# Performance work log

Hardware: AMD Instinct MI355X
Metric: run time of the kernel (lower is better)

## Reference

```python
import jax, jax.numpy as jnp
import numpy as np

NUM_CP = 64
D_MODEL = 128
N = 1_000_000


def setup_inputs() -> dict:
    key = jax.random.key(0)
    k_t, k_cp = jax.random.split(key)
    t = jax.random.uniform(k_t, (N,), dtype=jnp.float32)  # in [0,1)
    control_points = jax.random.normal(k_cp, (NUM_CP, D_MODEL), dtype=jnp.float32) / np.sqrt(NUM_CP)
    return {"t": t, "control_points": control_points}


def reference(t, control_points):
    # Faithful to the torch loop:
    #   out = sum_{i=0}^{K-2} (1 - |t - i|) * cp[i]
    # Note: weights are NOT clamped to >=0 in the original, so we keep the
    # dense (possibly negative) triangular weights and express the sum as a
    # single [N, K-1] @ [K-1, D] matmul.
    t = jnp.clip(t, 0.0, 1.0)                         # [N]
    k = control_points.shape[0] - 1                   # K-1 terms in the loop
    idx = jnp.arange(k, dtype=t.dtype)                # [K-1]
    weights = 1.0 - jnp.abs(t[:, None] - idx[None, :])  # [N, K-1]
    return weights @ control_points[:-1]              # [N, D]
```

## Files before the change

### kernel.cpp

```cpp
#include <hip/hip_runtime.h>

#define NUM_CP 64
#define D_MODEL 128

typedef float f32x4 __attribute__((ext_vector_type(4)));

__global__ __launch_bounds__(256) void spline_fused(const float* __restrict__ t,
                                                    const float* __restrict__ cp,
                                                    float* __restrict__ out, int n) {
    __shared__ float sbc[2 * D_MODEL];

    const int tid = threadIdx.x;
    if (tid < D_MODEL) {
        const int d = tid;
        float v0 = cp[d];
        float B = v0, C = -v0;
        for (int i = 1; i < NUM_CP - 1; ++i) {
            float v = cp[i * D_MODEL + d];
            B = fmaf(1.0f - (float)i, v, B);
            C += v;
        }
        sbc[d] = B;
        sbc[D_MODEL + d] = C;
    }
    __syncthreads();

    const int lane = tid & 63;
    const int c    = lane & 31;
    const int half = lane >> 5;

    const f32x4 b  = reinterpret_cast<const f32x4*>(sbc)[c];
    const f32x4 cv = reinterpret_cast<const f32x4*>(sbc + D_MODEL)[c];

    const int waveGlobal = blockIdx.x * 4 + (tid >> 6);
    const int nWaves     = gridDim.x * 4;
    const int rowStride  = nWaves * 8;
    f32x4* __restrict__ outq = reinterpret_cast<f32x4*>(out);

    for (int R0 = waveGlobal * 8; R0 < n; R0 += rowStride) {
        const int R = R0 + half * 4;
        if (R + 3 < n) {
            f32x4 t4 = *reinterpret_cast<const f32x4*>(t + R);
            float tv[4];
#pragma unroll
            for (int k = 0; k < 4; ++k) tv[k] = fminf(fmaxf(t4[k], 0.0f), 1.0f);
#pragma unroll
            for (int k = 0; k < 4; ++k) {
                f32x4 o;
                o.x = fmaf(tv[k], cv.x, b.x);
                o.y = fmaf(tv[k], cv.y, b.y);
                o.z = fmaf(tv[k], cv.z, b.z);
                o.w = fmaf(tv[k], cv.w, b.w);
                __builtin_nontemporal_store(o, &outq[(R + k) * 32 + c]);
            }
        } else {
            for (int k = 0; k < 4; ++k) {
                const int r = R + k;
                if (r < n) {
                    float tv = fminf(fmaxf(t[r], 0.0f), 1.0f);
                    f32x4 o;
                    o.x = fmaf(tv, cv.x, b.x);
                    o.y = fmaf(tv, cv.y, b.y);
                    o.z = fmaf(tv, cv.z, b.z);
                    o.w = fmaf(tv, cv.w, b.w);
                    __builtin_nontemporal_store(o, &outq[r * 32 + c]);
                }
            }
        }
    }
}

extern "C" void kernel_launch(void* const* d_in, const int* in_sizes, int n_in,
                              void* d_out, int out_size, void* d_ws, size_t ws_size,
                              hipStream_t stream) {
    const float* t  = (const float*)d_in[0];
    const float* cp = (const float*)d_in[1];
    float* out = (float*)d_out;
    const int n = in_sizes[0];

    const int waveTasks  = (n + 7) / 8;
    const int wantBlocks = (waveTasks + 3) / 4;
    const int blocks = wantBlocks < 2048 ? wantBlocks : 2048;
    spline_fused<<<blocks, 256, 0, stream>>>(t, cp, out, n);
}
```

Measured before the change: 103.5 us.

## Assign contiguous row chunks per block and stage t through LDS

Replaces the grid-stride loop with one contiguous chunk of rows per block (about 496 rows for this input, capped at 512). The block's slice of t is loaded cooperatively into shared memory, overlapping the control-point reduction before the barrier. This aims to improve write locality and to take the global t load off the per-wave store loop. The kernel is dominated by the large output write, so these changes touch only a small part of the cost, and the added shared buffer and barrier add some overhead.

```diff
diff --git a/kernel.cpp b/kernel.cpp
--- a/kernel.cpp
+++ b/kernel.cpp
@@ -2,45 +2,56 @@
 
 #define NUM_CP 64
 #define D_MODEL 128
+#define RPB_MAX 512
 
 typedef float f32x4 __attribute__((ext_vector_type(4)));
 
 __global__ __launch_bounds__(256) void spline_fused(const float* __restrict__ t,
                                                     const float* __restrict__ cp,
-                                                    float* __restrict__ out, int n) {
+                                                    float* __restrict__ out,
+                                                    int n, int rpb) {
     __shared__ float sbc[2 * D_MODEL];
+    __shared__ float st[RPB_MAX];
 
     const int tid = threadIdx.x;
+
     if (tid < D_MODEL) {
-        const int d = tid;
-        float v0 = cp[d];
+        float v0 = cp[tid];
         float B = v0, C = -v0;
         for (int i = 1; i < NUM_CP - 1; ++i) {
-            float v = cp[i * D_MODEL + d];
+            float v = cp[i * D_MODEL + tid];
             B = fmaf(1.0f - (float)i, v, B);
             C += v;
         }
-        sbc[d] = B;
-        sbc[D_MODEL + d] = C;
+        sbc[tid] = B;
+        sbc[D_MODEL + tid] = C;
+    }
+
+    const int base = blockIdx.x * rpb;
+    const int cnt  = min(rpb, n - base);
+    {
+        const f32x4* tq = reinterpret_cast<const f32x4*>(t + base);
+        const int quads = cnt >> 2;
+        for (int q = tid; q < quads; q += 256)
+            reinterpret_cast<f32x4*>(st)[q] = tq[q];
+        for (int r = (quads << 2) + tid; r < cnt; r += 256)
+            st[r] = t[base + r];
     }
     __syncthreads();
 
     const int lane = tid & 63;
     const int c    = lane & 31;
     const int half = lane >> 5;
+    const int wave = tid >> 6;
 
     const f32x4 b  = reinterpret_cast<const f32x4*>(sbc)[c];
     const f32x4 cv = reinterpret_cast<const f32x4*>(sbc + D_MODEL)[c];
+    f32x4* __restrict__ outq = reinterpret_cast<f32x4*>(out) + (size_t)base * (D_MODEL / 4);
 
-    const int waveGlobal = blockIdx.x * 4 + (tid >> 6);
-    const int nWaves     = gridDim.x * 4;
-    const int rowStride  = nWaves * 8;
-    f32x4* __restrict__ outq = reinterpret_cast<f32x4*>(out);
-
-    for (int R0 = waveGlobal * 8; R0 < n; R0 += rowStride) {
-        const int R = R0 + half * 4;
-        if (R + 3 < n) {
-            f32x4 t4 = *reinterpret_cast<const f32x4*>(t + R);
+    for (int r0 = wave * 8; r0 < cnt; r0 += 32) {
+        const int r = r0 + half * 4;
+        if (r0 + 7 < cnt) {
+            const f32x4 t4 = reinterpret_cast<const f32x4*>(st)[r >> 2];
             float tv[4];
 #pragma unroll
             for (int k = 0; k < 4; ++k) tv[k] = fminf(fmaxf(t4[k], 0.0f), 1.0f);
@@ -51,19 +62,19 @@
                 o.y = fmaf(tv[k], cv.y, b.y);
                 o.z = fmaf(tv[k], cv.z, b.z);
                 o.w = fmaf(tv[k], cv.w, b.w);
-                __builtin_nontemporal_store(o, &outq[(R + k) * 32 + c]);
+                __builtin_nontemporal_store(o, &outq[(r + k) * (D_MODEL / 4) + c]);
             }
         } else {
             for (int k = 0; k < 4; ++k) {
-                const int r = R + k;
-                if (r < n) {
-                    float tv = fminf(fmaxf(t[r], 0.0f), 1.0f);
+                const int rr = r + k;
+                if (rr < cnt) {
+                    const float tv = fminf(fmaxf(st[rr], 0.0f), 1.0f);
                     f32x4 o;
                     o.x = fmaf(tv, cv.x, b.x);
                     o.y = fmaf(tv, cv.y, b.y);
                     o.z = fmaf(tv, cv.z, b.z);
                     o.w = fmaf(tv, cv.w, b.w);
-                    __builtin_nontemporal_store(o, &outq[r * 32 + c]);
+                    __builtin_nontemporal_store(o, &outq[rr * (D_MODEL / 4) + c]);
                 }
             }
         }
@@ -78,8 +89,9 @@
     float* out = (float*)d_out;
     const int n = in_sizes[0];
 
-    const int waveTasks  = (n + 7) / 8;
-    const int wantBlocks = (waveTasks + 3) / 4;
-    const int blocks = wantBlocks < 2048 ? wantBlocks : 2048;
-    spline_fused<<<blocks, 256, 0, stream>>>(t, cp, out, n);
+    int rpb = ((n + 2048 * 8 - 1) / (2048 * 8)) * 8;
+    if (rpb > RPB_MAX) rpb = RPB_MAX;
+    if (rpb < 8) rpb = 8;
+    const int blocks = (n + rpb - 1) / rpb;
+    spline_fused<<<blocks, 256, 0, stream>>>(t, cp, out, n, rpb);
 }
```

Result: slower. 110.6 us (+6.8%).
